# Kernel optimization log

Hardware: AMD Instinct MI355X
Metric: run time of the kernel (lower is better)

## Reference

```python
import jax, jax.numpy as jnp
import numpy as np

DIM = 512
NUM_HEADS = 8
HEAD_DIM = DIM // NUM_HEADS
SCALE = HEAD_DIM ** -0.5
B, N, K_HOPS = 16, 1024, 5


def setup_inputs() -> dict:
    key = jax.random.key(0)
    ks = jax.random.split(key, 7)
    x = jax.random.normal(ks[0], (B, N, DIM), jnp.float32)
    Hstack = jax.random.uniform(ks[1], (K_HOPS, N, N), jnp.float32)
    hop_logits_attn = jax.random.normal(ks[2], (NUM_HEADS, K_HOPS), jnp.float32)
    rel_alpha = jax.random.normal(ks[3], (NUM_HEADS,), jnp.float32)
    Wqkv = jax.random.normal(ks[4], (3 * DIM, DIM), jnp.float32) * 0.02
    Wproj = jax.random.normal(ks[5], (DIM, DIM), jnp.float32) * 0.02
    bproj = jax.random.normal(ks[6], (DIM,), jnp.float32) * 0.02
    return {"x": x, "Hstack": Hstack, "hop_logits_attn": hop_logits_attn,
            "rel_alpha": rel_alpha, "Wqkv": Wqkv, "Wproj": Wproj, "bproj": bproj}


def reference(x, Hstack, hop_logits_attn, rel_alpha, Wqkv, Wproj, bproj):
    bs, n_tok, c_dim = x.shape
    # qkv projection: [B,N,3C] -> [3,B,H,N,hd]
    qkv = (x @ Wqkv.T).reshape(bs, n_tok, 3, NUM_HEADS, c_dim // NUM_HEADS)
    qkv = qkv.transpose(2, 0, 3, 1, 4)
    q, k, v = qkv[0], qkv[1], qkv[2]
    logits = jnp.einsum('bhnd,bhmd->bhnm', q, k) * SCALE  # [B,H,N,N]
    # hop-distance bias: per-head softmax mixture over K hop matrices
    w = jax.nn.softmax(hop_logits_attn, axis=-1)          # [H,K]
    B_head = jnp.einsum('hk,kij->hij', w, Hstack)          # [H,N,N]
    attn_bias = rel_alpha[:, None, None] * B_head          # [H,N,N]
    attn = jax.nn.softmax(logits + attn_bias[None], axis=-1)
    out = jnp.einsum('bhnm,bhmd->bhnd', attn, v)           # [B,H,N,hd]
    out = out.transpose(0, 2, 1, 3).reshape(bs, n_tok, c_dim)
    return out @ Wproj.T + bproj
```

## Files before the change

kernel.cpp:

```cpp
#include <hip/hip_runtime.h>
#include <hip/hip_bf16.h>
#include <hip/hip_fp16.h>
#include <stdint.h>

#define DIM   512
#define NH    8
#define HD    64
#define NB    16
#define NTOK  1024
#define KHOPS 5

typedef __attribute__((ext_vector_type(8))) short bf16x8;
typedef __attribute__((ext_vector_type(4))) float f32x4;

#define LOG2E 1.4426950408889634f

__device__ __forceinline__ unsigned short f32_to_bf16(float f) {
    unsigned int u = __builtin_bit_cast(unsigned int, f);
    unsigned int r = (u + 0x7FFFu + ((u >> 16) & 1u)) >> 16;
    return (unsigned short)r;
}

__device__ __forceinline__ float fast_exp2(float x) {
    return __builtin_amdgcn_exp2f(x);
}

#define AS1C(p) ((const __attribute__((address_space(1))) void*)(p))
#define AS3(p)  ((__attribute__((address_space(3))) void*)(p))

__global__ __launch_bounds__(256) void cvt_all(const float* __restrict__ x,
                                               const float* __restrict__ wq,
                                               const float* __restrict__ wp,
                                               unsigned short* __restrict__ xb,
                                               unsigned short* __restrict__ wqb,
                                               unsigned short* __restrict__ wpb) {
    int bid = blockIdx.x;
    const float* in; unsigned short* out; int i;
    if (bid < 8192)      { in = x;  out = xb;  i = bid * 256 + threadIdx.x; }
    else if (bid < 8960) { in = wq; out = wqb; i = (bid - 8192) * 256 + threadIdx.x; }
    else                 { in = wp; out = wpb; i = (bid - 8960) * 256 + threadIdx.x; }
    float4 v = reinterpret_cast<const float4*>(in)[i];
    ushort4 o;
    o.x = f32_to_bf16(v.x); o.y = f32_to_bf16(v.y);
    o.z = f32_to_bf16(v.z); o.w = f32_to_bf16(v.w);
    reinterpret_cast<ushort4*>(out)[i] = o;
}

__global__ __launch_bounds__(256) void bias_fused(const float* __restrict__ H,
                                                  const float* __restrict__ hop_logits,
                                                  const float* __restrict__ rel_alpha,
                                                  uint32_t* __restrict__ biast) {
    const int tid = threadIdx.x;
    const int jt = blockIdx.x, it = blockIdx.y;
    const int j0 = jt * 64, i0 = it * 64;
    float cf[NH][KHOPS];
#pragma unroll
    for (int h = 0; h < NH; ++h) {
        float m = -1e30f;
#pragma unroll
        for (int k = 0; k < KHOPS; ++k) m = fmaxf(m, hop_logits[h * KHOPS + k]);
        float s = 0.f;
#pragma unroll
        for (int k = 0; k < KHOPS; ++k) { cf[h][k] = fast_exp2((hop_logits[h * KHOPS + k] - m) * LOG2E); s += cf[h][k]; }
        float ra = rel_alpha[h] * LOG2E / s;
#pragma unroll
        for (int k = 0; k < KHOPS; ++k) cf[h][k] *= ra;
    }
    const int r = tid >> 2, c0 = (tid & 3) * 16;
    float hv[KHOPS][16];
#pragma unroll
    for (int k = 0; k < KHOPS; ++k) {
        const float4* src = reinterpret_cast<const float4*>(
            H + (size_t)k * 1048576 + (size_t)(i0 + r) * 1024 + j0 + c0);
#pragma unroll
        for (int q = 0; q < 4; ++q) {
            float4 v = src[q];
            hv[k][q * 4 + 0] = v.x; hv[k][q * 4 + 1] = v.y;
            hv[k][q * 4 + 2] = v.z; hv[k][q * 4 + 3] = v.w;
        }
    }
    for (int h = 0; h < NH; ++h) {
        uint32_t buf[8];
#pragma unroll
        for (int q = 0; q < 4; ++q) {
            float a0 = 0.f, a1 = 0.f, a2 = 0.f, a3 = 0.f;
#pragma unroll
            for (int k = 0; k < KHOPS; ++k) {
                a0 += cf[h][k] * hv[k][q * 4 + 0];
                a1 += cf[h][k] * hv[k][q * 4 + 1];
                a2 += cf[h][k] * hv[k][q * 4 + 2];
                a3 += cf[h][k] * hv[k][q * 4 + 3];
            }
            buf[q * 2 + 0] = __builtin_bit_cast(uint32_t, __floats2half2_rn(a0, a1));
            buf[q * 2 + 1] = __builtin_bit_cast(uint32_t, __floats2half2_rn(a2, a3));
        }
        uint32_t* dst = biast + ((size_t)h * 1024 + i0 + r) * 512 + ((j0 + c0) >> 1);
        uint4 w0; w0.x = buf[0]; w0.y = buf[1]; w0.z = buf[2]; w0.w = buf[3];
        uint4 w1; w1.x = buf[4]; w1.y = buf[5]; w1.z = buf[6]; w1.w = buf[7];
        reinterpret_cast<uint4*>(dst)[0] = w0;
        reinterpret_cast<uint4*>(dst)[1] = w1;
    }
}

__global__ __launch_bounds__(256) void gemm_qkv(const unsigned short* __restrict__ A,
                                                const unsigned short* __restrict__ Bw,
                                                unsigned short* __restrict__ qkv,
                                                unsigned short* __restrict__ vt) {
    __shared__ unsigned short As[128 * 32];
    __shared__ unsigned short Bs[128 * 32];
    const int tid  = threadIdx.x;
    const int lane = tid & 63;
    const int w    = tid >> 6;
    const int wr   = (w >> 1) * 64, wc = (w & 1) * 64;
    const int l15  = lane & 15, quad = lane >> 4;
    const int bid  = blockIdx.x;
    const int xcd  = bid & 7, slot = bid >> 3;
    const int m0   = (xcd * 16 + (slot & 15)) * 128;
    const int n0   = (slot >> 4) * 128;
    const int K = 512, Nn = 1536;

    f32x4 acc[4][4];
#pragma unroll
    for (int i = 0; i < 4; ++i)
#pragma unroll
        for (int j = 0; j < 4; ++j) { acc[i][j][0] = 0.f; acc[i][j][1] = 0.f; acc[i][j][2] = 0.f; acc[i][j][3] = 0.f; }

    for (int k0 = 0; k0 < K; k0 += 32) {
        __syncthreads();
#pragma unroll
        for (int t = 0; t < 2; ++t) {
            int c = t * 256 + w * 64 + lane;
            int r = c >> 2, kh = c & 3;
            const unsigned short* ga = A  + (size_t)(m0 + r) * K + k0 + kh * 8;
            const unsigned short* gb = Bw + (size_t)(n0 + r) * K + k0 + kh * 8;
            __builtin_amdgcn_global_load_lds(AS1C(ga), AS3(&As[(t * 256 + w * 64) * 8]), 16, 0, 0);
            __builtin_amdgcn_global_load_lds(AS1C(gb), AS3(&Bs[(t * 256 + w * 64) * 8]), 16, 0, 0);
        }
        __syncthreads();
        bf16x8 af[4], bfr[4];
#pragma unroll
        for (int rt = 0; rt < 4; ++rt)
            af[rt] = *reinterpret_cast<const bf16x8*>(&As[(wr + rt * 16 + l15) * 32 + quad * 8]);
#pragma unroll
        for (int ct = 0; ct < 4; ++ct)
            bfr[ct] = *reinterpret_cast<const bf16x8*>(&Bs[(wc + ct * 16 + l15) * 32 + quad * 8]);
#pragma unroll
        for (int rt = 0; rt < 4; ++rt)
#pragma unroll
            for (int ct = 0; ct < 4; ++ct)
                acc[rt][ct] = __builtin_amdgcn_mfma_f32_16x16x32_bf16(af[rt], bfr[ct], acc[rt][ct], 0, 0, 0);
    }

    if (n0 < 1024) {
#pragma unroll
        for (int rt = 0; rt < 4; ++rt)
#pragma unroll
            for (int ct = 0; ct < 4; ++ct)
#pragma unroll
                for (int reg = 0; reg < 4; ++reg) {
                    int row = m0 + wr + rt * 16 + quad * 4 + reg;
                    int col = n0 + wc + ct * 16 + l15;
                    qkv[(size_t)row * Nn + col] = f32_to_bf16(acc[rt][ct][reg]);
                }
    } else {
        const int b = m0 >> 10;
#pragma unroll
        for (int ct = 0; ct < 4; ++ct) {
            int c = n0 - 1024 + wc + ct * 16 + l15;
            unsigned short* vrow = vt + ((size_t)(b * 8) * 64 + c) * 1024;
#pragma unroll
            for (int rt = 0; rt < 4; ++rt) {
                int trow = (m0 & 1023) + wr + rt * 16 + quad * 4;
                ushort4 pk;
                pk.x = f32_to_bf16(acc[rt][ct][0]);
                pk.y = f32_to_bf16(acc[rt][ct][1]);
                pk.z = f32_to_bf16(acc[rt][ct][2]);
                pk.w = f32_to_bf16(acc[rt][ct][3]);
                *reinterpret_cast<ushort4*>(vrow + trow) = pk;
            }
        }
    }
}

__global__ __launch_bounds__(256) void gemm_proj(const unsigned short* __restrict__ A,
                                                 const unsigned short* __restrict__ Bw,
                                                 float* __restrict__ C,
                                                 const float* __restrict__ cbias) {
    __shared__ unsigned short As[128 * 32];
    __shared__ unsigned short Bs[128 * 32];
    const int tid  = threadIdx.x;
    const int lane = tid & 63;
    const int w    = tid >> 6;
    const int wr   = (w >> 1) * 64, wc = (w & 1) * 64;
    const int l15  = lane & 15, quad = lane >> 4;
    const int bid  = blockIdx.x;
    const int xcd  = bid & 7, slot = bid >> 3;
    const int m0   = (xcd * 16 + (slot & 15)) * 128;
    const int n0   = (slot >> 4) * 128;
    const int K = 512, Nn = 512;

    f32x4 acc[4][4];
#pragma unroll
    for (int i = 0; i < 4; ++i)
#pragma unroll
        for (int j = 0; j < 4; ++j) { acc[i][j][0] = 0.f; acc[i][j][1] = 0.f; acc[i][j][2] = 0.f; acc[i][j][3] = 0.f; }

    for (int k0 = 0; k0 < K; k0 += 32) {
        __syncthreads();
#pragma unroll
        for (int t = 0; t < 2; ++t) {
            int c = t * 256 + w * 64 + lane;
            int r = c >> 2, kh = c & 3;
            const unsigned short* ga = A  + (size_t)(m0 + r) * K + k0 + kh * 8;
            const unsigned short* gb = Bw + (size_t)(n0 + r) * K + k0 + kh * 8;
            __builtin_amdgcn_global_load_lds(AS1C(ga), AS3(&As[(t * 256 + w * 64) * 8]), 16, 0, 0);
            __builtin_amdgcn_global_load_lds(AS1C(gb), AS3(&Bs[(t * 256 + w * 64) * 8]), 16, 0, 0);
        }
        __syncthreads();
        bf16x8 af[4], bfr[4];
#pragma unroll
        for (int rt = 0; rt < 4; ++rt)
            af[rt] = *reinterpret_cast<const bf16x8*>(&As[(wr + rt * 16 + l15) * 32 + quad * 8]);
#pragma unroll
        for (int ct = 0; ct < 4; ++ct)
            bfr[ct] = *reinterpret_cast<const bf16x8*>(&Bs[(wc + ct * 16 + l15) * 32 + quad * 8]);
#pragma unroll
        for (int rt = 0; rt < 4; ++rt)
#pragma unroll
            for (int ct = 0; ct < 4; ++ct)
                acc[rt][ct] = __builtin_amdgcn_mfma_f32_16x16x32_bf16(af[rt], bfr[ct], acc[rt][ct], 0, 0, 0);
    }

#pragma unroll
    for (int ct = 0; ct < 4; ++ct) {
        int col = n0 + wc + ct * 16 + l15;
        float bv = cbias[col];
#pragma unroll
        for (int rt = 0; rt < 4; ++rt)
#pragma unroll
            for (int reg = 0; reg < 4; ++reg) {
                int row = m0 + wr + rt * 16 + quad * 4 + reg;
                C[(size_t)row * Nn + col] = acc[rt][ct][reg] + bv;
            }
    }
}

__global__ __launch_bounds__(512, 2) void flash_attn(const unsigned short* __restrict__ qkv,
                                                     const unsigned short* __restrict__ vt,
                                                     const uint32_t* __restrict__ biast,
                                                     unsigned short* __restrict__ aout) {
    __shared__ unsigned short Kb[2][64 * 64];
    __shared__ unsigned short Vb[2][64 * 64];
    __shared__ __align__(16) unsigned short Ps[8 * 32 * 64];
    const int tid  = threadIdx.x;
    const int lane = tid & 63, w = tid >> 6;
    const int l15  = lane & 15, quad = lane >> 4;
    const int h = blockIdx.x, qt = blockIdx.y, b = blockIdx.z;
    const int i0 = qt * 256 + w * 32;
    const float kscale = 0.125f * LOG2E;
    const int l7 = l15 & 7;
    const int psw = l7 << 3;

    bf16x8 qf[2][2];
#pragma unroll
    for (int rt = 0; rt < 2; ++rt)
#pragma unroll
        for (int ks = 0; ks < 2; ++ks)
            qf[rt][ks] = *reinterpret_cast<const bf16x8*>(
                qkv + (size_t)(b * 1024 + i0 + rt * 16 + l15) * 1536 + h * 64 + ks * 32 + quad * 8);

    f32x4 o[2][4];
    f32x4 lacc[2];
#pragma unroll
    for (int rt = 0; rt < 2; ++rt) {
#pragma unroll
        for (int nt = 0; nt < 4; ++nt) { o[rt][nt][0] = 0.f; o[rt][nt][1] = 0.f; o[rt][nt][2] = 0.f; o[rt][nt][3] = 0.f; }
        lacc[rt][0] = 0.f; lacc[rt][1] = 0.f; lacc[rt][2] = 0.f; lacc[rt][3] = 0.f;
    }

    bf16x8 ones;
#pragma unroll
    for (int e = 0; e < 8; ++e) ones[e] = (short)0x3F80;

    const int srow = lane >> 3;
    const int gch  = (lane & 7) ^ srow;
    const unsigned short* kgbase = qkv + (size_t)b * 1024 * 1536 + 512 + h * 64 + gch * 8;
    const unsigned short* vgbase = vt + (size_t)((b * 8 + h) * 64) * 1024 + gch * 8;
    const uint32_t* bb = biast + ((size_t)h * 1024 + i0) * 512;
    unsigned short* ps = &Ps[w * 32 * 64];

    {
        int rl = w * 8 + srow;
        __builtin_amdgcn_global_load_lds(AS1C(kgbase + (size_t)rl * 1536),
                                         AS3(&Kb[0][(w * 8) * 64]), 16, 0, 0);
        __builtin_amdgcn_global_load_lds(AS1C(vgbase + (size_t)rl * 1024),
                                         AS3(&Vb[0][(w * 8) * 64]), 16, 0, 0);
    }

#pragma unroll 2
    for (int it = 0; it < 16; ++it) {
        const int cur = it & 1, nxt = cur ^ 1;
        const int j0 = it * 64;
        __syncthreads();

        if (it < 15) {
            const int j0n = j0 + 64;
            int rl = w * 8 + srow;
            __builtin_amdgcn_global_load_lds(AS1C(kgbase + (size_t)(j0n + rl) * 1536),
                                             AS3(&Kb[nxt][(w * 8) * 64]), 16, 0, 0);
            __builtin_amdgcn_global_load_lds(AS1C(vgbase + (size_t)rl * 1024 + j0n),
                                             AS3(&Vb[nxt][(w * 8) * 64]), 16, 0, 0);
        }

        uint2 bl[2][4];
#pragma unroll
        for (int rt = 0; rt < 2; ++rt)
#pragma unroll
            for (int jt = 0; jt < 4; ++jt)
                bl[rt][jt] = *reinterpret_cast<const uint2*>(
                    bb + (size_t)(rt * 16 + l15) * 512 + (j0 >> 1) + jt * 8 + quad * 2);

        f32x4 s[2][4];
#pragma unroll
        for (int rt = 0; rt < 2; ++rt)
#pragma unroll
            for (int jt = 0; jt < 4; ++jt) { s[rt][jt][0] = 0.f; s[rt][jt][1] = 0.f; s[rt][jt][2] = 0.f; s[rt][jt][3] = 0.f; }
        __builtin_amdgcn_s_setprio(1);
#pragma unroll
        for (int ks = 0; ks < 2; ++ks) {
            bf16x8 kf[4];
#pragma unroll
            for (int jt = 0; jt < 4; ++jt)
                kf[jt] = *reinterpret_cast<const bf16x8*>(
                    &Kb[cur][(jt * 16 + l15) * 64 + (((ks * 4 + quad) ^ l7) * 8)]);
#pragma unroll
            for (int rt = 0; rt < 2; ++rt)
#pragma unroll
                for (int jt = 0; jt < 4; ++jt)
                    s[rt][jt] = __builtin_amdgcn_mfma_f32_16x16x32_bf16(kf[jt], qf[rt][ks], s[rt][jt], 0, 0, 0);
        }
        __builtin_amdgcn_s_setprio(0);

#pragma unroll
        for (int rt = 0; rt < 2; ++rt)
#pragma unroll
            for (int jt = 0; jt < 4; ++jt) {
                float2 f0 = __half22float2(__builtin_bit_cast(__half2, bl[rt][jt].x));
                float2 f1 = __half22float2(__builtin_bit_cast(__half2, bl[rt][jt].y));
                float p0 = fast_exp2(__builtin_fmaf(s[rt][jt][0], kscale, f0.x));
                float p1 = fast_exp2(__builtin_fmaf(s[rt][jt][1], kscale, f0.y));
                float p2 = fast_exp2(__builtin_fmaf(s[rt][jt][2], kscale, f1.x));
                float p3 = fast_exp2(__builtin_fmaf(s[rt][jt][3], kscale, f1.y));
                uint32_t u0 = (uint32_t)f32_to_bf16(p0) | ((uint32_t)f32_to_bf16(p1) << 16);
                uint32_t u1 = (uint32_t)f32_to_bf16(p2) | ((uint32_t)f32_to_bf16(p3) << 16);
                uint2 pk; pk.x = u0; pk.y = u1;
                *reinterpret_cast<uint2*>(
                    ps + (((rt * 16 + l15) * 64 + jt * 16 + quad * 4) ^ psw)) = pk;
            }

        __builtin_amdgcn_s_setprio(1);
#pragma unroll
        for (int ks = 0; ks < 2; ++ks) {
            bf16x8 pf[2], vf[4];
#pragma unroll
            for (int rt = 0; rt < 2; ++rt)
                pf[rt] = *reinterpret_cast<const bf16x8*>(
                    ps + (((rt * 16 + l15) * 64 + ks * 32 + quad * 8) ^ psw));
#pragma unroll
            for (int nt = 0; nt < 4; ++nt)
                vf[nt] = *reinterpret_cast<const bf16x8*>(
                    &Vb[cur][(nt * 16 + l15) * 64 + (((ks * 4 + quad) ^ l7) * 8)]);
#pragma unroll
            for (int rt = 0; rt < 2; ++rt) {
#pragma unroll
                for (int nt = 0; nt < 4; ++nt)
                    o[rt][nt] = __builtin_amdgcn_mfma_f32_16x16x32_bf16(pf[rt], vf[nt], o[rt][nt], 0, 0, 0);
                lacc[rt] = __builtin_amdgcn_mfma_f32_16x16x32_bf16(pf[rt], ones, lacc[rt], 0, 0, 0);
            }
        }
        __builtin_amdgcn_s_setprio(0);
    }

#pragma unroll
    for (int rt = 0; rt < 2; ++rt) {
        float inv[4];
#pragma unroll
        for (int reg = 0; reg < 4; ++reg) inv[reg] = 1.f / lacc[rt][reg];
#pragma unroll
        for (int nt = 0; nt < 4; ++nt)
#pragma unroll
            for (int reg = 0; reg < 4; ++reg) {
                int row = b * 1024 + i0 + rt * 16 + quad * 4 + reg;
                int col = h * 64 + nt * 16 + l15;
                aout[(size_t)row * 512 + col] = f32_to_bf16(o[rt][nt][reg] * inv[reg]);
            }
    }
}

extern "C" void kernel_launch(void* const* d_in, const int* in_sizes, int n_in,
                              void* d_out, int out_size, void* d_ws, size_t ws_size,
                              hipStream_t stream) {
    const float* x          = (const float*)d_in[0];
    const float* Hstack     = (const float*)d_in[1];
    const float* hop_logits = (const float*)d_in[2];
    const float* rel_alpha  = (const float*)d_in[3];
    const float* Wqkv       = (const float*)d_in[4];
    const float* Wproj      = (const float*)d_in[5];
    const float* bproj      = (const float*)d_in[6];
    float* out = (float*)d_out;

    char* ws = (char*)d_ws;
    unsigned short* xb    = (unsigned short*)(ws);
    unsigned short* wqb   = (unsigned short*)(ws + 16777216);
    unsigned short* wpb   = (unsigned short*)(ws + 18350080);
    unsigned short* qkvb  = (unsigned short*)(ws + 18874368);
    unsigned short* vtb   = (unsigned short*)(ws + 69206016);
    uint32_t*       biast = (uint32_t*)(ws + 85983232);
    unsigned short* aoutb = (unsigned short*)(ws + 102760448);

    cvt_all<<<9216, 256, 0, stream>>>(x, Wqkv, Wproj, xb, wqb, wpb);

    bias_fused<<<dim3(16, 16), 256, 0, stream>>>(Hstack, hop_logits, rel_alpha, biast);

    gemm_qkv<<<1536, 256, 0, stream>>>(xb, wqb, qkvb, vtb);

    flash_attn<<<dim3(8, 4, 16), 512, 0, stream>>>(qkvb, vtb, biast, aoutb);

    gemm_proj<<<512, 256, 0, stream>>>(aoutb, wpb, out, bproj);
}
```

Measured before the change: 275.5 us.

## Double-buffer GEMM LDS tiles and prefetch attention bias one iteration ahead

The QKV and output-projection GEMMs now use two LDS buffers. Each iteration issues the global-to-LDS loads for the next K-slice before running the MFMAs on the current one, and one barrier per iteration replaces two. The flash attention kernel loads the bias tile for the next key block into registers while the current block uses the tile loaded earlier, which hides global-load latency. The cost is double the LDS in the GEMMs and extra registers in attention, which could reduce occupancy.

```diff
diff --git a/kernel.cpp b/kernel.cpp
--- a/kernel.cpp
+++ b/kernel.cpp
@@ -106,8 +106,8 @@
                                                 const unsigned short* __restrict__ Bw,
                                                 unsigned short* __restrict__ qkv,
                                                 unsigned short* __restrict__ vt) {
-    __shared__ unsigned short As[128 * 32];
-    __shared__ unsigned short Bs[128 * 32];
+    __shared__ unsigned short As[2][128 * 32];
+    __shared__ unsigned short Bs[2][128 * 32];
     const int tid  = threadIdx.x;
     const int lane = tid & 63;
     const int w    = tid >> 6;
@@ -119,37 +119,48 @@
     const int n0   = (slot >> 4) * 128;
     const int K = 512, Nn = 1536;
 
+    const int sc = w * 64 + lane;
+    const int sr = sc >> 2, skh = sc & 3;
+    const unsigned short* gaB = A  + (size_t)(m0 + sr) * K + skh * 8;
+    const unsigned short* gbB = Bw + (size_t)(n0 + sr) * K + skh * 8;
+    const unsigned short* gaB2 = A  + (size_t)(m0 + 64 + sr) * K + skh * 8;
+    const unsigned short* gbB2 = Bw + (size_t)(n0 + 64 + sr) * K + skh * 8;
+
+#define STAGE_QKV(buf, k0s)                                                              \
+    do {                                                                                 \
+        __builtin_amdgcn_global_load_lds(AS1C(gaB  + (k0s)), AS3(&As[buf][sc * 8]), 16, 0, 0);          \
+        __builtin_amdgcn_global_load_lds(AS1C(gbB  + (k0s)), AS3(&Bs[buf][sc * 8]), 16, 0, 0);          \
+        __builtin_amdgcn_global_load_lds(AS1C(gaB2 + (k0s)), AS3(&As[buf][(256 + sc) * 8]), 16, 0, 0);  \
+        __builtin_amdgcn_global_load_lds(AS1C(gbB2 + (k0s)), AS3(&Bs[buf][(256 + sc) * 8]), 16, 0, 0);  \
+    } while (0)
+
     f32x4 acc[4][4];
 #pragma unroll
     for (int i = 0; i < 4; ++i)
 #pragma unroll
         for (int j = 0; j < 4; ++j) { acc[i][j][0] = 0.f; acc[i][j][1] = 0.f; acc[i][j][2] = 0.f; acc[i][j][3] = 0.f; }
 
+    STAGE_QKV(0, 0);
+    __syncthreads();
+    int cur = 0;
     for (int k0 = 0; k0 < K; k0 += 32) {
-        __syncthreads();
-#pragma unroll
-        for (int t = 0; t < 2; ++t) {
-            int c = t * 256 + w * 64 + lane;
-            int r = c >> 2, kh = c & 3;
-            const unsigned short* ga = A  + (size_t)(m0 + r) * K + k0 + kh * 8;
-            const unsigned short* gb = Bw + (size_t)(n0 + r) * K + k0 + kh * 8;
-            __builtin_amdgcn_global_load_lds(AS1C(ga), AS3(&As[(t * 256 + w * 64) * 8]), 16, 0, 0);
-            __builtin_amdgcn_global_load_lds(AS1C(gb), AS3(&Bs[(t * 256 + w * 64) * 8]), 16, 0, 0);
-        }
-        __syncthreads();
+        if (k0 + 32 < K) STAGE_QKV(cur ^ 1, k0 + 32);
         bf16x8 af[4], bfr[4];
 #pragma unroll
         for (int rt = 0; rt < 4; ++rt)
-            af[rt] = *reinterpret_cast<const bf16x8*>(&As[(wr + rt * 16 + l15) * 32 + quad * 8]);
+            af[rt] = *reinterpret_cast<const bf16x8*>(&As[cur][(wr + rt * 16 + l15) * 32 + quad * 8]);
 #pragma unroll
         for (int ct = 0; ct < 4; ++ct)
-            bfr[ct] = *reinterpret_cast<const bf16x8*>(&Bs[(wc + ct * 16 + l15) * 32 + quad * 8]);
+            bfr[ct] = *reinterpret_cast<const bf16x8*>(&Bs[cur][(wc + ct * 16 + l15) * 32 + quad * 8]);
 #pragma unroll
         for (int rt = 0; rt < 4; ++rt)
 #pragma unroll
             for (int ct = 0; ct < 4; ++ct)
                 acc[rt][ct] = __builtin_amdgcn_mfma_f32_16x16x32_bf16(af[rt], bfr[ct], acc[rt][ct], 0, 0, 0);
-    }
+        __syncthreads();
+        cur ^= 1;
+    }
+#undef STAGE_QKV
 
     if (n0 < 1024) {
 #pragma unroll
@@ -186,8 +197,8 @@
                                                  const unsigned short* __restrict__ Bw,
                                                  float* __restrict__ C,
                                                  const float* __restrict__ cbias) {
-    __shared__ unsigned short As[128 * 32];
-    __shared__ unsigned short Bs[128 * 32];
+    __shared__ unsigned short As[2][128 * 32];
+    __shared__ unsigned short Bs[2][128 * 32];
     const int tid  = threadIdx.x;
     const int lane = tid & 63;
     const int w    = tid >> 6;
@@ -199,37 +210,48 @@
     const int n0   = (slot >> 4) * 128;
     const int K = 512, Nn = 512;
 
+    const int sc = w * 64 + lane;
+    const int sr = sc >> 2, skh = sc & 3;
+    const unsigned short* gaB  = A  + (size_t)(m0 + sr) * K + skh * 8;
+    const unsigned short* gbB  = Bw + (size_t)(n0 + sr) * K + skh * 8;
+    const unsigned short* gaB2 = A  + (size_t)(m0 + 64 + sr) * K + skh * 8;
+    const unsigned short* gbB2 = Bw + (size_t)(n0 + 64 + sr) * K + skh * 8;
+
+#define STAGE_PRJ(buf, k0s)                                                              \
+    do {                                                                                 \
+        __builtin_amdgcn_global_load_lds(AS1C(gaB  + (k0s)), AS3(&As[buf][sc * 8]), 16, 0, 0);          \
+        __builtin_amdgcn_global_load_lds(AS1C(gbB  + (k0s)), AS3(&Bs[buf][sc * 8]), 16, 0, 0);          \
+        __builtin_amdgcn_global_load_lds(AS1C(gaB2 + (k0s)), AS3(&As[buf][(256 + sc) * 8]), 16, 0, 0);  \
+        __builtin_amdgcn_global_load_lds(AS1C(gbB2 + (k0s)), AS3(&Bs[buf][(256 + sc) * 8]), 16, 0, 0);  \
+    } while (0)
+
     f32x4 acc[4][4];
 #pragma unroll
     for (int i = 0; i < 4; ++i)
 #pragma unroll
         for (int j = 0; j < 4; ++j) { acc[i][j][0] = 0.f; acc[i][j][1] = 0.f; acc[i][j][2] = 0.f; acc[i][j][3] = 0.f; }
 
+    STAGE_PRJ(0, 0);
+    __syncthreads();
+    int cur = 0;
     for (int k0 = 0; k0 < K; k0 += 32) {
-        __syncthreads();
-#pragma unroll
-        for (int t = 0; t < 2; ++t) {
-            int c = t * 256 + w * 64 + lane;
-            int r = c >> 2, kh = c & 3;
-            const unsigned short* ga = A  + (size_t)(m0 + r) * K + k0 + kh * 8;
-            const unsigned short* gb = Bw + (size_t)(n0 + r) * K + k0 + kh * 8;
-            __builtin_amdgcn_global_load_lds(AS1C(ga), AS3(&As[(t * 256 + w * 64) * 8]), 16, 0, 0);
-            __builtin_amdgcn_global_load_lds(AS1C(gb), AS3(&Bs[(t * 256 + w * 64) * 8]), 16, 0, 0);
-        }
-        __syncthreads();
+        if (k0 + 32 < K) STAGE_PRJ(cur ^ 1, k0 + 32);
         bf16x8 af[4], bfr[4];
 #pragma unroll
         for (int rt = 0; rt < 4; ++rt)
-            af[rt] = *reinterpret_cast<const bf16x8*>(&As[(wr + rt * 16 + l15) * 32 + quad * 8]);
+            af[rt] = *reinterpret_cast<const bf16x8*>(&As[cur][(wr + rt * 16 + l15) * 32 + quad * 8]);
 #pragma unroll
         for (int ct = 0; ct < 4; ++ct)
-            bfr[ct] = *reinterpret_cast<const bf16x8*>(&Bs[(wc + ct * 16 + l15) * 32 + quad * 8]);
+            bfr[ct] = *reinterpret_cast<const bf16x8*>(&Bs[cur][(wc + ct * 16 + l15) * 32 + quad * 8]);
 #pragma unroll
         for (int rt = 0; rt < 4; ++rt)
 #pragma unroll
             for (int ct = 0; ct < 4; ++ct)
                 acc[rt][ct] = __builtin_amdgcn_mfma_f32_16x16x32_bf16(af[rt], bfr[ct], acc[rt][ct], 0, 0, 0);
-    }
+        __syncthreads();
+        cur ^= 1;
+    }
+#undef STAGE_PRJ
 
 #pragma unroll
     for (int ct = 0; ct < 4; ++ct) {
@@ -296,6 +318,13 @@
         __builtin_amdgcn_global_load_lds(AS1C(vgbase + (size_t)rl * 1024),
                                          AS3(&Vb[0][(w * 8) * 64]), 16, 0, 0);
     }
+    uint2 blc[2][4];
+#pragma unroll
+    for (int rt = 0; rt < 2; ++rt)
+#pragma unroll
+        for (int jt = 0; jt < 4; ++jt)
+            blc[rt][jt] = *reinterpret_cast<const uint2*>(
+                bb + (size_t)(rt * 16 + l15) * 512 + jt * 8 + quad * 2);
 
 #pragma unroll 2
     for (int it = 0; it < 16; ++it) {
@@ -312,13 +341,14 @@
                                              AS3(&Vb[nxt][(w * 8) * 64]), 16, 0, 0);
         }
 
-        uint2 bl[2][4];
+        const int j0p = (it < 15) ? ((j0 + 64) >> 1) : 0;
+        uint2 bln[2][4];
 #pragma unroll
         for (int rt = 0; rt < 2; ++rt)
 #pragma unroll
             for (int jt = 0; jt < 4; ++jt)
-                bl[rt][jt] = *reinterpret_cast<const uint2*>(
-                    bb + (size_t)(rt * 16 + l15) * 512 + (j0 >> 1) + jt * 8 + quad * 2);
+                bln[rt][jt] = *reinterpret_cast<const uint2*>(
+                    bb + (size_t)(rt * 16 + l15) * 512 + j0p + jt * 8 + quad * 2);
 
         f32x4 s[2][4];
 #pragma unroll
@@ -345,8 +375,8 @@
         for (int rt = 0; rt < 2; ++rt)
 #pragma unroll
             for (int jt = 0; jt < 4; ++jt) {
-                float2 f0 = __half22float2(__builtin_bit_cast(__half2, bl[rt][jt].x));
-                float2 f1 = __half22float2(__builtin_bit_cast(__half2, bl[rt][jt].y));
+                float2 f0 = __half22float2(__builtin_bit_cast(__half2, blc[rt][jt].x));
+                float2 f1 = __half22float2(__builtin_bit_cast(__half2, blc[rt][jt].y));
                 float p0 = fast_exp2(__builtin_fmaf(s[rt][jt][0], kscale, f0.x));
                 float p1 = fast_exp2(__builtin_fmaf(s[rt][jt][1], kscale, f0.y));
                 float p2 = fast_exp2(__builtin_fmaf(s[rt][jt][2], kscale, f1.x));
@@ -379,6 +409,12 @@
             }
         }
         __builtin_amdgcn_s_setprio(0);
+
+#pragma unroll
+        for (int rt = 0; rt < 2; ++rt)
+#pragma unroll
+            for (int jt = 0; jt < 4; ++jt)
+                blc[rt][jt] = bln[rt][jt];
     }
 
 #pragma unroll
```

Measured after the change: 305.7 us. 10.9% more time.
